# Kernel tuning notes

Measured on AMD Instinct MI355X. Metric: run time of the kernel, lower is better.

The kernel has to match this reference:

```python
import jax, jax.numpy as jnp
import numpy as np

N_NODES = 100000
N_EDGES = 1600000
IN_DIM = 128
HID = 128
OUT_DIM = 64
N_LAYERS = 2
MAXK = 16


def setup_inputs() -> dict:
    key = jax.random.key(0)
    ks = jax.random.split(key, 8)
    x = jax.random.normal(ks[0], (N_NODES, IN_DIM), dtype=jnp.float32)
    src = jax.random.randint(ks[1], (N_EDGES,), 0, N_NODES, dtype=jnp.int32)
    dst = jax.random.randint(ks[2], (N_EDGES,), 0, N_NODES, dtype=jnp.int32)
    # Linear weights stored as [in, out] (y = x @ W + b), xavier-like scale
    s_in = float(np.sqrt(2.0 / (IN_DIM + HID)))
    s_h = float(np.sqrt(2.0 / (HID + HID)))
    s_out = float(np.sqrt(2.0 / (HID + OUT_DIM)))
    W_in = jax.random.normal(ks[3], (IN_DIM, HID), dtype=jnp.float32) * s_in
    b_in = jnp.zeros((HID,), dtype=jnp.float32)
    W_lin = jax.random.normal(ks[4], (N_LAYERS, HID, HID), dtype=jnp.float32) * s_h
    b_lin = jnp.zeros((N_LAYERS, HID), dtype=jnp.float32)
    eps = jnp.zeros((N_LAYERS,), dtype=jnp.float32)  # learn_eps=True, init_eps=0
    W_out = jax.random.normal(ks[5], (HID, OUT_DIM), dtype=jnp.float32) * s_out
    b_out = jnp.zeros((OUT_DIM,), dtype=jnp.float32)
    return {"x": x, "src": src, "dst": dst, "W_in": W_in, "b_in": b_in,
            "W_lin": W_lin, "b_lin": b_lin, "eps": eps,
            "W_out": W_out, "b_out": b_out}


def _maxk(x, k):
    # OPTMaxK: keep top-k entries per row (dim=1), zero the rest.
    _, idx = jax.lax.top_k(x, k)                      # [N, k]
    rows = jnp.arange(x.shape[0])[:, None]            # [N, 1]
    mask = jnp.zeros_like(x).at[rows, idx].set(1.0)
    return x * mask


def reference(x, src, dst, W_in, b_in, W_lin, b_lin, eps, W_out, b_out):
    n = x.shape[0]
    h = jax.nn.relu(x @ W_in + b_in)                  # lin_in + relu
    for i in range(N_LAYERS):
        h = h @ W_lin[i] + b_lin[i]                   # per-layer Linear
        h_sparse = _maxk(h, MAXK)                     # MaxK nonlinearity (dropout p=0 -> identity)
        # GIN sum aggregation over edges: neigh[v] = sum_{(u->v)} h_sparse[u]
        msg = jnp.take(h_sparse, src, axis=0)         # [E, HID] irregular gather
        neigh = jax.ops.segment_sum(msg, dst, num_segments=n)
        h = (1.0 + eps[i]) * h_sparse + neigh         # eps residual (apply_func=None, no norm)
    return h @ W_out + b_out
```

## Files before the change

kernel.cpp:

```cpp
#include <hip/hip_runtime.h>
#include <cstdint>
#include <cstddef>


typedef __attribute__((ext_vector_type(8))) short bf16x8;
typedef __attribute__((ext_vector_type(4))) float f32x4;

#define BSHIFT 8
#define NBUK 512

__device__ __forceinline__ unsigned rne_bf16(float v) {
  unsigned u = __float_as_uint(v);
  return (u + 0x7fffu + ((u >> 16) & 1u)) >> 16;
}

__global__ __launch_bounds__(256) void wt_build_all_kernel(
    const float* __restrict__ W_in, const float* __restrict__ W_lin,
    const float* __restrict__ W_out, short* __restrict__ out) {
  const int i = blockIdx.x * 256 + threadIdx.x;
  if (i >= 57344) return;
  const float* W;
  int nout, local;
  short* H;
  if (i < 16384) {
    W = W_in; nout = 128; local = i; H = out;
  } else if (i < 32768) {
    W = W_lin; nout = 128; local = i - 16384; H = out + 32768;
  } else if (i < 49152) {
    W = W_lin + 16384; nout = 128; local = i - 32768; H = out + 65536;
  } else {
    W = W_out; nout = 64; local = i - 49152; H = out + 98304;
  }
  const int nn = local >> 7, k = local & 127;
  const float v = W[k * nout + nn];
  const unsigned hb = rne_bf16(v);
  const float hf = __uint_as_float(hb << 16);
  const unsigned lb = rne_bf16(v - hf);
  H[local] = (short)hb;
  H[local + nout * 128] = (short)lb;
}

__global__ __launch_bounds__(256, 2) void gemm_in_kernel(
    const float* __restrict__ X, const short* __restrict__ WtH,
    const short* __restrict__ WtL, const float* __restrict__ bias,
    short* __restrict__ Yh, short* __restrict__ Yl, int nrows, int ntiles) {
  constexpr int NOUT = 128;
  constexpr int NT = NOUT / 16;
  constexpr int LDB = 128 * 2 + 16;
  constexpr int PLANE = NOUT * LDB;
  __shared__ char lds[2 * PLANE];

  const int tid = threadIdx.x;
  for (int u = tid; u < 2 * NOUT * 16; u += 256) {
    const int plane = u / (NOUT * 16);
    const int v = u % (NOUT * 16);
    const int nrow = v >> 4, seg = v & 15;
    const short* src = plane ? WtL : WtH;
    const float4 d = *(const float4*)&src[nrow * 128 + seg * 8];
    *(float4*)&lds[plane * PLANE + nrow * LDB + seg * 16] = d;
  }
  __syncthreads();

  const int lane = tid & 63;
  const int wv = tid >> 6;
  const int li = lane & 15;
  const int kg = lane >> 4;

  float bv[NT];
#pragma unroll
  for (int t = 0; t < NT; ++t) bv[t] = bias[t * 16 + li];

  for (int tile = blockIdx.x; tile < ntiles; tile += gridDim.x) {
    const int rowbase = tile * 256 + wv * 64;

    f32x4 acc[4][NT];
#pragma unroll
    for (int rg = 0; rg < 4; ++rg)
#pragma unroll
      for (int t = 0; t < NT; ++t) acc[rg][t] = (f32x4){0.f, 0.f, 0.f, 0.f};

#pragma unroll
    for (int c = 0; c < 4; ++c) {
      bf16x8 ah[4], al[4];
#pragma unroll
      for (int rg = 0; rg < 4; ++rg) {
        const int row = rowbase + rg * 16 + li;
        const int rowc = (row < nrows) ? row : (nrows - 1);
        const float* xrow = X + (size_t)rowc * 128 + c * 32 + kg * 8;
        const float4 p0 = *(const float4*)&xrow[0];
        const float4 p1 = *(const float4*)&xrow[4];
        const float f[8] = {p0.x, p0.y, p0.z, p0.w, p1.x, p1.y, p1.z, p1.w};
#pragma unroll
        for (int e = 0; e < 8; ++e) {
          const unsigned hb = rne_bf16(f[e]);
          const float hf = __uint_as_float(hb << 16);
          ah[rg][e] = (short)hb;
          al[rg][e] = (short)rne_bf16(f[e] - hf);
        }
      }
      const int kb = c * 64 + kg * 16;
#pragma unroll
      for (int t = 0; t < NT; ++t) {
        const int boff = (t * 16 + li) * LDB + kb;
        const bf16x8 bh = *(const bf16x8*)&lds[boff];
        const bf16x8 bl = *(const bf16x8*)&lds[PLANE + boff];
#pragma unroll
        for (int rg = 0; rg < 4; ++rg) {
          acc[rg][t] =
              __builtin_amdgcn_mfma_f32_16x16x32_bf16(al[rg], bh, acc[rg][t], 0, 0, 0);
          acc[rg][t] =
              __builtin_amdgcn_mfma_f32_16x16x32_bf16(ah[rg], bl, acc[rg][t], 0, 0, 0);
          acc[rg][t] =
              __builtin_amdgcn_mfma_f32_16x16x32_bf16(ah[rg], bh, acc[rg][t], 0, 0, 0);
        }
      }
    }

#pragma unroll
    for (int rg = 0; rg < 4; ++rg) {
      const int orow = rowbase + rg * 16 + kg * 4;
#pragma unroll
      for (int t = 0; t < NT; ++t) {
        const int col = t * 16 + li;
#pragma unroll
        for (int r = 0; r < 4; ++r) {
          const int rr = orow + r;
          if (rr < nrows) {
            const float o = fmaxf(acc[rg][t][r] + bv[t], 0.f);
            const unsigned hb = rne_bf16(o);
            const float hf = __uint_as_float(hb << 16);
            Yh[(size_t)rr * 128 + col] = (short)hb;
            Yl[(size_t)rr * 128 + col] = (short)rne_bf16(o - hf);
          }
        }
      }
    }
  }
}

template <int NOUT>
__global__ __launch_bounds__(256, 2) void gemm_pl_kernel(
    const short* __restrict__ Xh, const short* __restrict__ Xl,
    const short* __restrict__ WtH, const short* __restrict__ WtL,
    const float* __restrict__ bias, float* __restrict__ Y, int nrows,
    int ntiles) {
  constexpr int NT = NOUT / 16;
  constexpr int LDB = 128 * 2 + 16;
  constexpr int PLANE = NOUT * LDB;
  __shared__ char lds[2 * PLANE];

  const int tid = threadIdx.x;
  for (int u = tid; u < 2 * NOUT * 16; u += 256) {
    const int plane = u / (NOUT * 16);
    const int v = u % (NOUT * 16);
    const int nrow = v >> 4, seg = v & 15;
    const short* src = plane ? WtL : WtH;
    const float4 d = *(const float4*)&src[nrow * 128 + seg * 8];
    *(float4*)&lds[plane * PLANE + nrow * LDB + seg * 16] = d;
  }
  __syncthreads();

  const int lane = tid & 63;
  const int wv = tid >> 6;
  const int li = lane & 15;
  const int kg = lane >> 4;

  float bv[NT];
#pragma unroll
  for (int t = 0; t < NT; ++t) bv[t] = bias[t * 16 + li];

  for (int tile = blockIdx.x; tile < ntiles; tile += gridDim.x) {
    const int rowbase = tile * 256 + wv * 64;

    f32x4 acc[4][NT];
#pragma unroll
    for (int rg = 0; rg < 4; ++rg)
#pragma unroll
      for (int t = 0; t < NT; ++t) acc[rg][t] = (f32x4){0.f, 0.f, 0.f, 0.f};

#pragma unroll
    for (int c = 0; c < 4; ++c) {
      bf16x8 ah[4], al[4];
#pragma unroll
      for (int rg = 0; rg < 4; ++rg) {
        const int row = rowbase + rg * 16 + li;
        const int rowc = (row < nrows) ? row : (nrows - 1);
        ah[rg] = *(const bf16x8*)&Xh[(size_t)rowc * 128 + c * 32 + kg * 8];
        al[rg] = *(const bf16x8*)&Xl[(size_t)rowc * 128 + c * 32 + kg * 8];
      }
      const int kb = c * 64 + kg * 16;
#pragma unroll
      for (int t = 0; t < NT; ++t) {
        const int boff = (t * 16 + li) * LDB + kb;
        const bf16x8 bh = *(const bf16x8*)&lds[boff];
        const bf16x8 bl = *(const bf16x8*)&lds[PLANE + boff];
#pragma unroll
        for (int rg = 0; rg < 4; ++rg) {
          acc[rg][t] =
              __builtin_amdgcn_mfma_f32_16x16x32_bf16(al[rg], bh, acc[rg][t], 0, 0, 0);
          acc[rg][t] =
              __builtin_amdgcn_mfma_f32_16x16x32_bf16(ah[rg], bl, acc[rg][t], 0, 0, 0);
          acc[rg][t] =
              __builtin_amdgcn_mfma_f32_16x16x32_bf16(ah[rg], bh, acc[rg][t], 0, 0, 0);
        }
      }
    }

#pragma unroll
    for (int rg = 0; rg < 4; ++rg) {
      const int orow = rowbase + rg * 16 + kg * 4;
#pragma unroll
      for (int t = 0; t < NT; ++t) {
        const int col = t * 16 + li;
#pragma unroll
        for (int r = 0; r < 4; ++r) {
          const int rr = orow + r;
          if (rr < nrows) Y[(size_t)rr * NOUT + col] = acc[rg][t][r] + bv[t];
        }
      }
    }
  }
}

__global__ __launch_bounds__(256) void maxk_kernel(
    const float* __restrict__ T, unsigned char* __restrict__ Cs,
    float* __restrict__ Vs, int nrows) {
  const int lane = threadIdx.x & 63;
  const int wid = threadIdx.x >> 6;
  const unsigned long long below = ((unsigned long long)1 << lane) - 1;

  for (int row = blockIdx.x * 4 + wid; row < nrows; row += gridDim.x * 4) {
    const float o0 = T[(size_t)row * 128 + lane];
    const float o1 = T[(size_t)row * 128 + 64 + lane];
    const unsigned u0 = __float_as_uint(o0);
    const unsigned u1 = __float_as_uint(o1);
    const unsigned k0 = u0 ^ (((unsigned)((int)u0 >> 31)) | 0x80000000u);
    const unsigned k1 = u1 ^ (((unsigned)((int)u1 >> 31)) | 0x80000000u);

    unsigned P = 0;
    int kth = 16;
#pragma unroll
    for (int b = 31; b >= 0; --b) {
      const unsigned long long ball0 = __ballot(((k0 ^ P) >> b) == 1u);
      const unsigned long long ball1 = __ballot(((k1 ^ P) >> b) == 1u);
      const int c = __popcll(ball0) + __popcll(ball1);
      if (c >= kth)
        P |= (1u << b);
      else
        kth -= c;
    }
    const bool gt0 = k0 > P, gt1 = k1 > P;
    const unsigned long long g0 = __ballot(gt0);
    const unsigned long long g1 = __ballot(gt1);
    const int need = 16 - __popcll(g0) - __popcll(g1);
    const unsigned long long e0 = __ballot(k0 == P);
    const unsigned long long e1 = __ballot(k1 == P);
    const int need1 = need - __popcll(e0);
    const bool s0 = gt0 || (((e0 >> lane) & 1) &&
                            ((int)__popcll(e0 & below) < need));
    const bool s1 = gt1 || (((e1 >> lane) & 1) &&
                            ((int)__popcll(e1 & below) < need1));
    const unsigned long long m0 = __ballot(s0);
    const unsigned long long m1 = __ballot(s1);

    const int p0 = __popcll(m0 & below);
    const int p1 = __popcll(m0) + __popcll(m1 & below);
    if (s0) {
      Vs[(size_t)row * 16 + p0] = o0;
      Cs[(size_t)row * 16 + p0] = (unsigned char)lane;
    }
    if (s1) {
      Vs[(size_t)row * 16 + p1] = o1;
      Cs[(size_t)row * 16 + p1] = (unsigned char)(lane + 64);
    }
  }
}

__global__ __launch_bounds__(256) void bhist_kernel(const int* __restrict__ dst,
                                                    int* __restrict__ BC,
                                                    int E) {
  __shared__ int bh[NBUK];
  for (int i = threadIdx.x; i < NBUK; i += 256) bh[i] = 0;
  __syncthreads();
  const int stride = gridDim.x * 256;
  for (int e = blockIdx.x * 256 + threadIdx.x; e < E; e += stride)
    atomicAdd(&bh[dst[e] >> BSHIFT], 1);
  __syncthreads();
  for (int i = threadIdx.x; i < NBUK; i += 256)
    if (bh[i]) atomicAdd(&BC[i], bh[i]);
}

__global__ __launch_bounds__(NBUK) void bscan_kernel(
    const int* __restrict__ BC, int* __restrict__ bases,
    int* __restrict__ bcur, int* __restrict__ rs, int n, int E) {
  __shared__ int sc[NBUK];
  const int t = threadIdx.x;
  const int c = BC[t];
  sc[t] = c;
  __syncthreads();
  for (int st = 1; st < NBUK; st <<= 1) {
    const int v = sc[t];
    const int u = (t >= st) ? sc[t - st] : 0;
    __syncthreads();
    sc[t] = v + u;
    __syncthreads();
  }
  const int excl = sc[t] - c;
  bases[t] = excl;
  bcur[t] = excl;
  if (t == 0) rs[n] = E;
}

__global__ __launch_bounds__(256) void bin_kernel(
    const int* __restrict__ src, const int* __restrict__ dst,
    int* __restrict__ bcur, uint2* __restrict__ binned, int E, int chunk) {
  __shared__ int cnt[NBUK], off[NBUK], gbase[NBUK];
  __shared__ unsigned short bktof[4096];
  __shared__ uint2 buf[4096];
  const int t = threadIdx.x;
  const int beg = blockIdx.x * chunk;
  const int m = min(chunk, E - beg);
  if (m <= 0) return;

  for (int i = t; i < NBUK; i += 256) cnt[i] = 0;
  __syncthreads();

  int d[16], s[16], lp[16], bk[16];
#pragma unroll
  for (int i = 0; i < 16; ++i) {
    const int j = i * 256 + t;
    if (j < m) {
      d[i] = dst[beg + j];
      s[i] = src[beg + j];
      bk[i] = d[i] >> BSHIFT;
      lp[i] = atomicAdd(&cnt[bk[i]], 1);
    } else {
      bk[i] = -1;
    }
  }
  __syncthreads();

  for (int i = t; i < NBUK; i += 256) off[i] = cnt[i];
  __syncthreads();
  for (int st = 1; st < NBUK; st <<= 1) {
    int v0, v1, u0, u1;
    {
      const int i0 = t, i1 = t + 256;
      v0 = off[i0]; u0 = (i0 >= st) ? off[i0 - st] : 0;
      v1 = off[i1]; u1 = (i1 >= st) ? off[i1 - st] : 0;
    }
    __syncthreads();
    off[t] = v0 + u0;
    off[t + 256] = v1 + u1;
    __syncthreads();
  }

  for (int i = t; i < NBUK; i += 256) {
    const int c = cnt[i];
    if (c > 0) {
      gbase[i] = atomicAdd(&bcur[i], c);
      const int e0 = off[i] - c;
      for (int k = 0; k < c; ++k) bktof[e0 + k] = (unsigned short)i;
    }
  }
  __syncthreads();

#pragma unroll
  for (int i = 0; i < 16; ++i) {
    if (bk[i] >= 0) {
      buf[(off[bk[i]] - cnt[bk[i]]) + lp[i]] =
          make_uint2((unsigned)d[i], (unsigned)s[i]);
    }
  }
  __syncthreads();

  for (int j = t; j < m; j += 256) {
    const int b = bktof[j];
    const int e0 = off[b] - cnt[b];
    binned[gbase[b] + (j - e0)] = buf[j];
  }
}

__global__ __launch_bounds__(256) void bbuild_kernel(
    const int* __restrict__ bases, const int* __restrict__ BC,
    const uint2* __restrict__ binned, int* __restrict__ rs,
    int* __restrict__ csr_src, int n) {
  __shared__ int nd[256], sc[256], cur[256];
  const int b = blockIdx.x;
  const int t = threadIdx.x;
  const int base = bases[b];
  const int count = BC[b];
  const int node0 = b << BSHIFT;

  nd[t] = 0;
  __syncthreads();
  for (int i = t; i < count; i += 256)
    atomicAdd(&nd[binned[base + i].x & 255], 1);
  __syncthreads();

  sc[t] = nd[t];
  __syncthreads();
  for (int st = 1; st < 256; st <<= 1) {
    const int v = sc[t];
    const int u = (t >= st) ? sc[t - st] : 0;
    __syncthreads();
    sc[t] = v + u;
    __syncthreads();
  }
  const int excl = sc[t] - nd[t];
  cur[t] = excl;
  if (node0 + t < n) rs[node0 + t] = base + excl;
  __syncthreads();

  for (int i = t; i < count; i += 256) {
    const uint2 p = binned[base + i];
    const int pos = atomicAdd(&cur[p.x & 255], 1);
    csr_src[base + pos] = (int)p.y;
  }
}

__global__ __launch_bounds__(256) void gather6_kernel(
    const int* __restrict__ rs, const int* __restrict__ csr_src,
    const unsigned char* __restrict__ Cs, const float* __restrict__ Vs,
    const float* __restrict__ eps_p, short* __restrict__ Ah,
    short* __restrict__ Al, int nrows) {
  __shared__ __align__(16) float sv[4][16][16];
  __shared__ __align__(16) unsigned char scb[4][16][16];
  __shared__ float accb[4][4 * 132];
  const int lane = threadIdx.x & 63;
  const int wid = threadIdx.x >> 6;
  const float e1 = 1.0f + *eps_p;
  const int ee = lane >> 2;
  const int q = lane & 3;
  const int g = lane >> 4;
  const int p = lane & 15;
  float* acc = accb[wid];
  float4* acc4 = (float4*)acc;

  for (int r = blockIdx.x * 4 + wid; r < nrows; r += gridDim.x * 4) {
    for (int i = lane; i < 132; i += 64)
      acc4[i] = make_float4(0.f, 0.f, 0.f, 0.f);

    const int beg = rs[r], end = rs[r + 1];
    for (int base = beg; base < end; base += 16) {
      const int cnt = min(16, end - base);
      if (ee < cnt) {
        const int s = csr_src[base + ee];
        if (q == 0) {
          const int4 c4 = *(const int4*)&Cs[(size_t)s * 16];
          *(int4*)&scb[wid][ee][0] = c4;
        }
        const float4 v = *(const float4*)&Vs[(size_t)s * 16 + q * 4];
        *(float4*)&sv[wid][ee][q * 4] = v;
      }
      for (int e = 0; e < cnt; e += 4) {
        const int eg = e + g;
        if (eg < cnt) {
          const int col = scb[wid][eg][p];
          const float val = sv[wid][eg][p];
          acc[g * 132 + col] += val;
        }
      }
    }
    if (lane < 16) {
      const int c = Cs[(size_t)r * 16 + lane];
      const float v = Vs[(size_t)r * 16 + lane];
      acc[c] += e1 * v;
    }
    const float a0 = acc[lane] + acc[132 + lane] + acc[264 + lane] +
                     acc[396 + lane];
    const float a1 = acc[64 + lane] + acc[132 + 64 + lane] +
                     acc[264 + 64 + lane] + acc[396 + 64 + lane];
    const unsigned h0 = rne_bf16(a0);
    const unsigned h1 = rne_bf16(a1);
    Ah[(size_t)r * 128 + lane] = (short)h0;
    Ah[(size_t)r * 128 + 64 + lane] = (short)h1;
    Al[(size_t)r * 128 + lane] =
        (short)rne_bf16(a0 - __uint_as_float(h0 << 16));
    Al[(size_t)r * 128 + 64 + lane] =
        (short)rne_bf16(a1 - __uint_as_float(h1 << 16));
  }
}

extern "C" void kernel_launch(void* const* d_in, const int* in_sizes, int n_in,
                              void* d_out, int out_size, void* d_ws,
                              size_t ws_size, hipStream_t stream) {
  const float* x = (const float*)d_in[0];
  const int* src = (const int*)d_in[1];
  const int* dst = (const int*)d_in[2];
  const float* W_in = (const float*)d_in[3];
  const float* b_in = (const float*)d_in[4];
  const float* W_lin = (const float*)d_in[5];
  const float* b_lin = (const float*)d_in[6];
  const float* eps = (const float*)d_in[7];
  const float* W_out = (const float*)d_in[8];
  const float* b_out = (const float*)d_in[9];
  float* out = (float*)d_out;

  const int n = in_sizes[0] / 128;
  const int E = in_sizes[1];

  char* w = (char*)d_ws;
  float* B = (float*)w;               w += (size_t)n * 128 * 4;
  unsigned char* Cs = (unsigned char*)w; w += (size_t)n * 16;
  float* Vs = (float*)w;              w += (size_t)n * 16 * 4;
  int* rs = (int*)w;                  w += (size_t)(n + 1) * 4;
  int* csr_src = (int*)w;             w += (size_t)E * 4;
  uint2* binned = (uint2*)w;          w += (size_t)E * 8;
  int* BC = (int*)w;                  w += NBUK * 4;
  int* bases = (int*)w;               w += NBUK * 4;
  int* bcur = (int*)w;                w += NBUK * 4;
  short* wtAll = (short*)w;           w += (size_t)114688 * 2;
  short* Ah = (short*)w;              w += (size_t)n * 128 * 2;
  short* Al = (short*)w;              w += (size_t)n * 128 * 2;

  short* wtIn = wtAll;
  short* wtL0 = wtAll + 32768;
  short* wtL1 = wtAll + 65536;
  short* wtOut = wtAll + 98304;

  const int ptiles = (n + 255) / 256;
  const int nbuk_eff = (n + 255) >> BSHIFT;
  const int chunk = 4000;
  const int cblocks = (E + chunk - 1) / chunk;
  const dim3 blk(256);

  hipMemsetAsync(BC, 0, NBUK * 4, stream);
  bhist_kernel<<<256, blk, 0, stream>>>(dst, BC, E);
  bscan_kernel<<<1, NBUK, 0, stream>>>(BC, bases, bcur, rs, n, E);
  bin_kernel<<<cblocks, blk, 0, stream>>>(src, dst, bcur, binned, E, chunk);
  bbuild_kernel<<<nbuk_eff, blk, 0, stream>>>(bases, BC, binned, rs, csr_src,
                                              n);

  wt_build_all_kernel<<<(57344 + 255) / 256, blk, 0, stream>>>(W_in, W_lin,
                                                               W_out, wtAll);

  gemm_in_kernel<<<ptiles, blk, 0, stream>>>(x, wtIn, wtIn + 16384, b_in, Ah,
                                             Al, n, ptiles);

  for (int l = 0; l < 2; ++l) {
    short* wt = l ? wtL1 : wtL0;
    gemm_pl_kernel<128><<<ptiles, blk, 0, stream>>>(
        Ah, Al, wt, wt + 16384, b_lin + (size_t)l * 128, B, n, ptiles);
    maxk_kernel<<<2048, blk, 0, stream>>>(B, Cs, Vs, n);
    gather6_kernel<<<2048, blk, 0, stream>>>(rs, csr_src, Cs, Vs, eps + l, Ah,
                                             Al, n);
  }

  gemm_pl_kernel<64><<<ptiles, blk, 0, stream>>>(Ah, Al, wtOut, wtOut + 8192,
                                                 b_out, out, n, ptiles);
}
```

Measured before the change: 407.1 us.

## Process four rows per wavefront in maxk with early-exit radix select

```diff
diff --git a/kernel.cpp b/kernel.cpp
--- a/kernel.cpp
+++ b/kernel.cpp
@@ -227,51 +227,77 @@
     float* __restrict__ Vs, int nrows) {
   const int lane = threadIdx.x & 63;
   const int wid = threadIdx.x >> 6;
-  const unsigned long long below = ((unsigned long long)1 << lane) - 1;
-
-  for (int row = blockIdx.x * 4 + wid; row < nrows; row += gridDim.x * 4) {
-    const float o0 = T[(size_t)row * 128 + lane];
-    const float o1 = T[(size_t)row * 128 + 64 + lane];
-    const unsigned u0 = __float_as_uint(o0);
-    const unsigned u1 = __float_as_uint(o1);
-    const unsigned k0 = u0 ^ (((unsigned)((int)u0 >> 31)) | 0x80000000u);
-    const unsigned k1 = u1 ^ (((unsigned)((int)u1 >> 31)) | 0x80000000u);
+  const int sub = lane >> 4;
+  const int s = lane & 15;
+  const int shift = sub * 16;
+  const unsigned below = (1u << s) - 1u;
+  const int nquads = (nrows + 3) / 4;
+
+  for (int quad = blockIdx.x * 4 + wid; quad < nquads; quad += gridDim.x * 4) {
+    const int row = quad * 4 + sub;
+    const int rowc = (row < nrows) ? row : (nrows - 1);
+    const float* Trow = T + (size_t)rowc * 128;
+
+    float v[8];
+    unsigned k[8];
+#pragma unroll
+    for (int j = 0; j < 8; ++j) {
+      v[j] = Trow[j * 16 + s];
+      const unsigned u = __float_as_uint(v[j]);
+      k[j] = u ^ (((unsigned)((int)u >> 31)) | 0x80000000u);
+    }
 
     unsigned P = 0;
     int kth = 16;
-#pragma unroll
+    int sz = 128;
+    bool done = false;
     for (int b = 31; b >= 0; --b) {
-      const unsigned long long ball0 = __ballot(((k0 ^ P) >> b) == 1u);
-      const unsigned long long ball1 = __ballot(((k1 ^ P) >> b) == 1u);
-      const int c = __popcll(ball0) + __popcll(ball1);
-      if (c >= kth)
-        P |= (1u << b);
-      else
-        kth -= c;
-    }
-    const bool gt0 = k0 > P, gt1 = k1 > P;
-    const unsigned long long g0 = __ballot(gt0);
-    const unsigned long long g1 = __ballot(gt1);
-    const int need = 16 - __popcll(g0) - __popcll(g1);
-    const unsigned long long e0 = __ballot(k0 == P);
-    const unsigned long long e1 = __ballot(k1 == P);
-    const int need1 = need - __popcll(e0);
-    const bool s0 = gt0 || (((e0 >> lane) & 1) &&
-                            ((int)__popcll(e0 & below) < need));
-    const bool s1 = gt1 || (((e1 >> lane) & 1) &&
-                            ((int)__popcll(e1 & below) < need1));
-    const unsigned long long m0 = __ballot(s0);
-    const unsigned long long m1 = __ballot(s1);
-
-    const int p0 = __popcll(m0 & below);
-    const int p1 = __popcll(m0) + __popcll(m1 & below);
-    if (s0) {
-      Vs[(size_t)row * 16 + p0] = o0;
-      Cs[(size_t)row * 16 + p0] = (unsigned char)lane;
-    }
-    if (s1) {
-      Vs[(size_t)row * 16 + p1] = o1;
-      Cs[(size_t)row * 16 + p1] = (unsigned char)(lane + 64);
+      const unsigned tgt = (P >> b) | 1u;
+      int c = 0;
+#pragma unroll
+      for (int j = 0; j < 8; ++j) {
+        const unsigned long long bal = __ballot((k[j] >> b) == tgt);
+        c += __popc((unsigned)((bal >> shift) & 0xFFFFull));
+      }
+      if (!done) {
+        if (c >= kth) {
+          P |= (1u << b);
+          sz = c;
+        } else {
+          sz -= c;
+          kth -= c;
+        }
+        done = (sz == kth);
+      }
+      if (__all(done)) break;
+    }
+    if (done) P -= 1u;
+
+    unsigned gtm[8], eqm[8];
+    int gt_total = 0;
+#pragma unroll
+    for (int j = 0; j < 8; ++j) {
+      const unsigned long long gb = __ballot(k[j] > P);
+      const unsigned long long eb = __ballot(k[j] == P);
+      gtm[j] = (unsigned)((gb >> shift) & 0xFFFFull);
+      eqm[j] = (unsigned)((eb >> shift) & 0xFFFFull);
+      gt_total += __popc(gtm[j]);
+    }
+    const int need = 16 - gt_total;
+    int gt_pre = 0, eq_pre = 0;
+#pragma unroll
+    for (int j = 0; j < 8; ++j) {
+      const bool isgt = k[j] > P;
+      const bool iseq = k[j] == P;
+      const int gtb = gt_pre + __popc(gtm[j] & below);
+      const int eqb = eq_pre + __popc(eqm[j] & below);
+      if (row < nrows && (isgt || (iseq && eqb < need))) {
+        const int rank = gtb + (isgt ? min(eqb, need) : eqb);
+        Vs[(size_t)row * 16 + rank] = v[j];
+        Cs[(size_t)row * 16 + rank] = (unsigned char)(j * 16 + s);
+      }
+      gt_pre += __popc(gtm[j]);
+      eq_pre += __popc(eqm[j]);
     }
   }
 }
```

Result: faster. 393.8 us (-3.3%).
